# Kernel optimization log

Hardware: AMD Instinct MI355X
Metric: run time of the kernel (lower is better)

## Reference

```python
import jax, jax.numpy as jnp
import numpy as np

N_NODES = 100000
N_EDGES = 1600000
DIM = 128
N_LAYERS = 3   # num_gc_layers
N_RES = 3      # residual VQ layers
N_CODE = 16    # codebook_size
N_GRAPHS = 512
BN_EPS = 1e-5
COMMIT_W = 0.25


def _l2norm(v):
    return v * jax.lax.rsqrt(jnp.sum(v * v, axis=-1, keepdims=True) + 1e-12)


def setup_inputs() -> dict:
    key = jax.random.key(0)
    ks = jax.random.split(key, 8)
    s = 0.05
    x = jax.random.normal(ks[0], (N_NODES, DIM), jnp.float32)
    edge_index = jax.random.randint(ks[1], (2, N_EDGES), 0, N_NODES)
    batch = jnp.sort(jax.random.randint(ks[2], (N_NODES,), 0, N_GRAPHS))
    W1 = jax.random.normal(ks[3], (N_LAYERS, DIM, DIM), jnp.float32) * s
    b1 = jnp.zeros((N_LAYERS, DIM), jnp.float32)
    W2 = jax.random.normal(ks[4], (N_LAYERS, DIM, DIM), jnp.float32) * s
    b2 = jnp.zeros((N_LAYERS, DIM), jnp.float32)
    gamma = jnp.ones((N_LAYERS, DIM), jnp.float32)
    beta = jnp.zeros((N_LAYERS, DIM), jnp.float32)
    codebooks = jax.random.normal(ks[5], (N_LAYERS, N_RES, N_CODE, DIM), jnp.float32)
    return dict(x=x, edge_index=edge_index, batch=batch, W1=W1, b1=b1,
                W2=W2, b2=b2, gamma=gamma, beta=beta, codebooks=codebooks)


def reference(x, edge_index, batch, W1, b1, W2, b2, gamma, beta, codebooks):
    src, dst = edge_index[0], edge_index[1]
    h = x
    xs, ids = [], []
    commit_loss = jnp.float32(0.0)
    for i in range(N_LAYERS):
        # GINConv, eps=0: MLP((1+eps)*x + sum_{j->i} x_j)
        agg = jax.ops.segment_sum(h[src], dst, num_segments=N_NODES)
        h = agg + h
        h = jax.nn.relu(h @ W1[i] + b1[i]) @ W2[i] + b2[i]  # Linear-ReLU-Linear
        h = jax.nn.relu(h)                                   # outer F.relu
        # BatchNorm1d (training-mode batch stats, biased variance)
        mean = jnp.mean(h, axis=0)
        var = jnp.var(h, axis=0)
        h = (h - mean) * jax.lax.rsqrt(var + BN_EPS) * gamma[i] + beta[i]
        xs.append(h)
        # Residual VQ with cosine-sim codebook (3 residual layers)
        r = h
        lids = []
        for l in range(N_RES):
            cbn = _l2norm(codebooks[i, l])           # [K, D] normalized codebook
            sim = _l2norm(r) @ cbn.T                  # [N, K] cosine similarity
            idx = jnp.argmax(sim, axis=-1)            # nearest code
            q = cbn[idx]                              # quantized residual
            commit_loss = commit_loss + COMMIT_W * jnp.mean(
                (jax.lax.stop_gradient(q) - r) ** 2)
            r = r - jax.lax.stop_gradient(q)
            lids.append(idx)
        ids.append(jnp.stack(lids, axis=1))           # [N, N_RES]
    xs_cat = jnp.concatenate(xs, axis=1)              # [N, DIM*N_LAYERS]
    xpool = jax.ops.segment_sum(xs_cat, batch, num_segments=N_GRAPHS)
    id_cat = jnp.concatenate(ids, axis=1)             # [N, N_RES*N_LAYERS]
    return xpool, xs_cat, commit_loss, id_cat
```

## Files before the change

kernel.cpp:

```cpp
#include <hip/hip_runtime.h>
#include <hip/hip_bf16.h>

#define N_NODES 100000
#define N_EDGES 1600000
#define DIM 128
#define NLAY 3
#define NRES 3
#define NCODE 16
#define NGRAPH 512
#define SCAN_NB ((N_NODES + 255) / 256)
#define GEMM_NB ((N_NODES + 63) / 64)

using bf16 = __hip_bfloat16;

__device__ inline void atomAddD(double* p, double v) { unsafeAtomicAdd(p, v); }

__device__ inline double ldx(const void* p, long i, int isbf) {
  if (isbf) return (double)__bfloat162float(((const bf16*)p)[i]);
  return (double)((const float*)p)[i];
}
__device__ inline void stout(void* p, long i, double v, int isbf) {
  if (isbf) ((bf16*)p)[i] = __float2bfloat16((float)v);
  else ((float*)p)[i] = (float)v;
}

__global__ void k_detect(const unsigned int* __restrict__ x, int* __restrict__ flag) {
  int tid = threadIdx.x;
  int cnt = 0;
  for (int j = tid; j < 1024; j += 256) {
    unsigned int u = x[j];
    int e = (u >> 7) & 0xFF;
    cnt += (e >= 100 && e <= 135) ? 1 : 0;
  }
  __shared__ int sh[256];
  sh[tid] = cnt; __syncthreads();
  for (int s = 128; s; s >>= 1) { if (tid < s) sh[tid] += sh[tid + s]; __syncthreads(); }
  if (tid == 0) flag[0] = (sh[0] > 512) ? 1 : 0;
}

__global__ __launch_bounds__(256) void k_convert_f(const void* __restrict__ x, float* __restrict__ hf,
                                                   long n, const int* __restrict__ flag) {
  int isbf = flag[0];
  long i = (long)blockIdx.x * 256 + threadIdx.x;
  if (i < n) hf[i] = (float)ldx(x, i, isbf);
}

__global__ __launch_bounds__(256) void k_hist(const int* __restrict__ ei, int* __restrict__ deg) {
  int e = blockIdx.x * 256 + threadIdx.x;
  if (e < N_EDGES) atomicAdd(&deg[ei[N_EDGES + e]], 1);
}

__global__ __launch_bounds__(256) void k_scan1(const int* __restrict__ deg, int* __restrict__ bsum) {
  int i = blockIdx.x * 256 + threadIdx.x;
  int v = (i < N_NODES) ? deg[i] : 0;
  for (int o = 32; o; o >>= 1) v += __shfl_xor(v, o);
  __shared__ int sh[4];
  if ((threadIdx.x & 63) == 0) sh[threadIdx.x >> 6] = v;
  __syncthreads();
  if (threadIdx.x == 0) bsum[blockIdx.x] = sh[0] + sh[1] + sh[2] + sh[3];
}

__global__ void k_scan2(int* __restrict__ bsum) {
  __shared__ int sh[512];
  int t = threadIdx.x;
  int v = (t < SCAN_NB) ? bsum[t] : 0;
  sh[t] = v; __syncthreads();
  for (int s = 1; s < 512; s <<= 1) {
    int add = (t >= s) ? sh[t - s] : 0;
    __syncthreads();
    sh[t] += add;
    __syncthreads();
  }
  if (t < SCAN_NB) bsum[t] = sh[t] - v;
}

__global__ __launch_bounds__(256) void k_scan3(const int* __restrict__ deg, const int* __restrict__ bsum,
                                               int* __restrict__ ofs, int* __restrict__ cursor) {
  int t = threadIdx.x;
  int i = blockIdx.x * 256 + t;
  int v = (i < N_NODES) ? deg[i] : 0;
  __shared__ int sh[256];
  sh[t] = v; __syncthreads();
  for (int s = 1; s < 256; s <<= 1) {
    int add = (t >= s) ? sh[t - s] : 0;
    __syncthreads();
    sh[t] += add;
    __syncthreads();
  }
  int excl = sh[t] - v + bsum[blockIdx.x];
  if (i < N_NODES) { ofs[i] = excl; cursor[i] = excl; }
  if (i == N_NODES - 1) ofs[N_NODES] = excl + v;
}

__global__ __launch_bounds__(256) void k_fill(const int* __restrict__ ei, int* __restrict__ cursor,
                                              int* __restrict__ csr) {
  int e = blockIdx.x * 256 + threadIdx.x;
  if (e < N_EDGES) {
    int d = ei[N_EDGES + e];
    int p = atomicAdd(&cursor[d], 1);
    csr[p] = ei[e];
  }
}

__global__ __launch_bounds__(256) void k_gather(const float* __restrict__ hf,
                                                const int* __restrict__ ofs,
                                                const int* __restrict__ csr,
                                                float* __restrict__ outQ) {
  int node = blockIdx.x * 4 + (threadIdx.x >> 6);
  int lane = threadIdx.x & 63;
  int beg = ofs[node], end = ofs[node + 1];
  float2 sv = *(const float2*)&hf[(long)node * DIM + lane * 2];
  double accx = (double)sv.x, accy = (double)sv.y;
  int j = beg;
  for (; j + 3 < end; j += 4) {
    int s0 = csr[j], s1 = csr[j + 1], s2 = csr[j + 2], s3 = csr[j + 3];
    float2 v0 = *(const float2*)&hf[(long)s0 * DIM + lane * 2];
    float2 v1 = *(const float2*)&hf[(long)s1 * DIM + lane * 2];
    float2 v2 = *(const float2*)&hf[(long)s2 * DIM + lane * 2];
    float2 v3 = *(const float2*)&hf[(long)s3 * DIM + lane * 2];
    accx += (double)v0.x; accy += (double)v0.y;
    accx += (double)v1.x; accy += (double)v1.y;
    accx += (double)v2.x; accy += (double)v2.y;
    accx += (double)v3.x; accy += (double)v3.y;
  }
  for (; j < end; j++) {
    int s0 = csr[j];
    float2 v0 = *(const float2*)&hf[(long)s0 * DIM + lane * 2];
    accx += (double)v0.x; accy += (double)v0.y;
  }
  *(float2*)&outQ[(long)node * DIM + lane * 2] = make_float2((float)accx, (float)accy);
}

__global__ void k_cbn(const void* __restrict__ cb, double* __restrict__ cbn, const int* __restrict__ flag) {
  int isbf = flag[0];
  int b = blockIdx.x, d = threadIdx.x;
  double v0 = ldx(cb, (long)b * DIM + d, isbf);
  double v1 = ldx(cb, (long)b * DIM + d + 64, isbf);
  double ss = v0 * v0 + v1 * v1;
  for (int o = 32; o; o >>= 1) ss += __shfl_xor(ss, o);
  double inv = 1.0 / sqrt(ss + 1e-12);
  cbn[b * DIM + d] = v0 * inv;
  cbn[b * DIM + d + 64] = v1 * inv;
}

__global__ void k_gram(const double* __restrict__ cbn, double* __restrict__ G) {
  int b = blockIdx.x, t = threadIdx.x;
  int l = b / (48 * 48); int rem = b % (48 * 48); int a = rem / 48, c = rem % 48;
  const double* ra = cbn + (long)(l * 48 + a) * DIM;
  const double* rc = cbn + (long)(l * 48 + c) * DIM;
  double s = ra[t] * rc[t] + ra[t + 64] * rc[t + 64];
  for (int o = 32; o; o >>= 1) s += __shfl_xor(s, o);
  if (t == 0) G[b] = s;
}

__global__ __launch_bounds__(256) void k_gemm_relu_f(const float* __restrict__ in,
                                                     const float* __restrict__ W,
                                                     const float* __restrict__ bias,
                                                     float* __restrict__ out) {
  __shared__ float ul[64 * DIM];
  int tid = threadIdx.x;
  long base = (long)blockIdx.x * 64;
  for (int j = tid; j < 64 * DIM / 4; j += 256) {
    long row = base + (j >> 5);
    float4 v = make_float4(0.f, 0.f, 0.f, 0.f);
    if (row < N_NODES) v = *(const float4*)&in[base * DIM + (long)j * 4];
    *(float4*)&ul[j * 4] = v;
  }
  __syncthreads();
  int cl = tid & 31;
  int rw = tid >> 5;
  int c0 = cl * 4;
  float acc[8][4] = {};
  for (int k = 0; k < DIM; k += 4) {
    float4 w0 = *(const float4*)&W[(k + 0) * DIM + c0];
    float4 w1 = *(const float4*)&W[(k + 1) * DIM + c0];
    float4 w2 = *(const float4*)&W[(k + 2) * DIM + c0];
    float4 w3 = *(const float4*)&W[(k + 3) * DIM + c0];
#pragma unroll
    for (int r = 0; r < 8; r++) {
      float4 u = *(const float4*)&ul[(rw * 8 + r) * DIM + k];
      acc[r][0] += u.x * w0.x + u.y * w1.x + u.z * w2.x + u.w * w3.x;
      acc[r][1] += u.x * w0.y + u.y * w1.y + u.z * w2.y + u.w * w3.y;
      acc[r][2] += u.x * w0.z + u.y * w1.z + u.z * w2.z + u.w * w3.z;
      acc[r][3] += u.x * w0.w + u.y * w1.w + u.z * w2.w + u.w * w3.w;
    }
  }
  float4 bv = *(const float4*)&bias[c0];
#pragma unroll
  for (int r = 0; r < 8; r++) {
    long row = base + rw * 8 + r;
    if (row < N_NODES) {
      float4 o;
      o.x = fmaxf(acc[r][0] + bv.x, 0.f);
      o.y = fmaxf(acc[r][1] + bv.y, 0.f);
      o.z = fmaxf(acc[r][2] + bv.z, 0.f);
      o.w = fmaxf(acc[r][3] + bv.w, 0.f);
      *(float4*)&out[row * DIM + c0] = o;
    }
  }
}

__global__ __launch_bounds__(256) void k_gemm_relu_stats(const float* __restrict__ in,
                                                         const float* __restrict__ W,
                                                         const float* __restrict__ bias,
                                                         float* __restrict__ out,
                                                         double* __restrict__ stats8) {
  __shared__ __align__(16) float ul[64 * DIM];
  int tid = threadIdx.x;
  long base = (long)blockIdx.x * 64;
  for (int j = tid; j < 64 * DIM / 4; j += 256) {
    long row = base + (j >> 5);
    float4 v = make_float4(0.f, 0.f, 0.f, 0.f);
    if (row < N_NODES) v = *(const float4*)&in[base * DIM + (long)j * 4];
    *(float4*)&ul[j * 4] = v;
  }
  __syncthreads();
  int cl = tid & 31;
  int rw = tid >> 5;
  int c0 = cl * 4;
  float acc[8][4] = {};
  for (int k = 0; k < DIM; k += 4) {
    float4 w0 = *(const float4*)&W[(k + 0) * DIM + c0];
    float4 w1 = *(const float4*)&W[(k + 1) * DIM + c0];
    float4 w2 = *(const float4*)&W[(k + 2) * DIM + c0];
    float4 w3 = *(const float4*)&W[(k + 3) * DIM + c0];
#pragma unroll
    for (int r = 0; r < 8; r++) {
      float4 u = *(const float4*)&ul[(rw * 8 + r) * DIM + k];
      acc[r][0] += u.x * w0.x + u.y * w1.x + u.z * w2.x + u.w * w3.x;
      acc[r][1] += u.x * w0.y + u.y * w1.y + u.z * w2.y + u.w * w3.y;
      acc[r][2] += u.x * w0.z + u.y * w1.z + u.z * w2.z + u.w * w3.z;
      acc[r][3] += u.x * w0.w + u.y * w1.w + u.z * w2.w + u.w * w3.w;
    }
  }
  float4 bv = *(const float4*)&bias[c0];
  double cs0 = 0.0, cs1 = 0.0, cs2 = 0.0, cs3 = 0.0;
  double q0 = 0.0, q1 = 0.0, q2 = 0.0, q3 = 0.0;
#pragma unroll
  for (int r = 0; r < 8; r++) {
    long row = base + rw * 8 + r;
    if (row < N_NODES) {
      float4 o;
      o.x = fmaxf(acc[r][0] + bv.x, 0.f);
      o.y = fmaxf(acc[r][1] + bv.y, 0.f);
      o.z = fmaxf(acc[r][2] + bv.z, 0.f);
      o.w = fmaxf(acc[r][3] + bv.w, 0.f);
      *(float4*)&out[row * DIM + c0] = o;
      double dx = (double)o.x, dy = (double)o.y, dz = (double)o.z, dw = (double)o.w;
      cs0 += dx; q0 += dx * dx;
      cs1 += dy; q1 += dy * dy;
      cs2 += dz; q2 += dz * dz;
      cs3 += dw; q3 += dw * dw;
    }
  }
  __syncthreads();
  double* sred = (double*)ul;
  sred[rw * 128 + c0 + 0] = cs0; sred[1024 + rw * 128 + c0 + 0] = q0;
  sred[rw * 128 + c0 + 1] = cs1; sred[1024 + rw * 128 + c0 + 1] = q1;
  sred[rw * 128 + c0 + 2] = cs2; sred[1024 + rw * 128 + c0 + 2] = q2;
  sred[rw * 128 + c0 + 3] = cs3; sred[1024 + rw * 128 + c0 + 3] = q3;
  __syncthreads();
  if (tid < 128) {
    double S = 0.0, S2 = 0.0;
#pragma unroll
    for (int i = 0; i < 8; i++) { S += sred[i * 128 + tid]; S2 += sred[1024 + i * 128 + tid]; }
    int slab = blockIdx.x & 7;
    atomAddD(&stats8[slab * 256 + tid], S);
    atomAddD(&stats8[slab * 256 + 128 + tid], S2);
  }
}

__global__ __launch_bounds__(256) void k_post(float* __restrict__ h,
                                              const double* __restrict__ stats8,
                                              const void* __restrict__ gamma,
                                              const void* __restrict__ beta,
                                              const int* __restrict__ batch,
                                              void* __restrict__ out,
                                              double* __restrict__ xpool,
                                              double* __restrict__ hh,
                                              int l, const int* __restrict__ flag) {
  __shared__ float hl[64 * 132];
  __shared__ double hq[64 * 4];
  __shared__ double ssl[256];
  __shared__ int sbat[64];
  int isbf = flag[0];
  int tid = threadIdx.x;
  long base = (long)blockIdx.x * 64;
  if (tid < 128) {
    double sum = 0.0, sumsq = 0.0;
#pragma unroll
    for (int s8 = 0; s8 < 8; s8++) { sum += stats8[s8 * 256 + tid]; sumsq += stats8[s8 * 256 + 128 + tid]; }
    double mean = sum / (double)N_NODES;
    double var = sumsq / (double)N_NODES - mean * mean;
    double sc = ldx(gamma, (long)l * DIM + tid, isbf) / sqrt(var + 1e-5);
    ssl[tid] = sc;
    ssl[DIM + tid] = ldx(beta, (long)l * DIM + tid, isbf) - mean * sc;
  }
  if (tid < 64) {
    long row = base + tid;
    sbat[tid] = (row < N_NODES) ? batch[row] : -1;
  }
  __syncthreads();
  int d = tid & 127, half = tid >> 7;
  double sc = ssl[d], sh = ssl[DIM + d];
  const long XS_BASE = (long)NGRAPH * DIM * NLAY;
  for (int rr = half; rr < 64; rr += 2) {
    long row = base + rr;
    float vf = 0.f;
    if (row < N_NODES) {
      double v = (double)h[row * DIM + d] * sc + sh;
      vf = (float)v;
      h[row * DIM + d] = vf;
      stout(out, XS_BASE + row * (DIM * NLAY) + l * DIM + d, v, isbf);
    }
    hl[rr * 132 + d] = vf;
  }
  __syncthreads();
  {
    int row = tid >> 2, q = tid & 3;
    double s2 = 0.0;
    const float* hp = &hl[row * 132 + q * 32];
#pragma unroll
    for (int i = 0; i < 32; i++) { double v = (double)hp[i]; s2 += v * v; }
    hq[row * 4 + q] = s2;
  }
  __syncthreads();
  if (tid < 64) {
    long n = base + tid;
    if (n < N_NODES) hh[n] = hq[tid * 4] + hq[tid * 4 + 1] + hq[tid * 4 + 2] + hq[tid * 4 + 3];
  } else if (tid >= 128) {
    int dd = tid - 128;
    int g = sbat[0];
    double acc = 0.0;
    for (int r = 0; r < 64; r++) {
      int gg = sbat[r];
      if (gg < 0) break;
      if (gg != g) {
        atomAddD(&xpool[(long)g * (DIM * NLAY) + l * DIM + dd], acc);
        acc = 0.0; g = gg;
      }
      acc += (double)hl[r * 132 + dd];
    }
    atomAddD(&xpool[(long)g * (DIM * NLAY) + l * DIM + dd], acc);
  }
}

__global__ __launch_bounds__(256) void k_dotH(const float* __restrict__ hn,
                                              const double* __restrict__ cbnL,
                                              float* __restrict__ dH) {
  __shared__ double cl[48 * 134];
  int tid = threadIdx.x;
  for (int j = tid; j < 48 * DIM; j += 256) { int c = j >> 7, k = j & 127; cl[c * 134 + k] = cbnL[j]; }
  __syncthreads();
  int ct = tid & 7; int c0 = ct * 6; int rt = tid >> 3;
  long r0 = (long)blockIdx.x * 64 + rt; long r1 = r0 + 32;
  long r0c = r0 < N_NODES ? r0 : (N_NODES - 1);
  long r1c = r1 < N_NODES ? r1 : (N_NODES - 1);
  double acc0[6] = {}, acc1[6] = {};
  for (int k = 0; k < DIM; k += 4) {
    float4 h0 = *(const float4*)&hn[r0c * DIM + k];
    float4 h1 = *(const float4*)&hn[r1c * DIM + k];
#pragma unroll
    for (int j = 0; j < 6; j++) {
      double2 ca = *(const double2*)&cl[(c0 + j) * 134 + k];
      double2 cb = *(const double2*)&cl[(c0 + j) * 134 + k + 2];
      acc0[j] += (double)h0.x * ca.x + (double)h0.y * ca.y + (double)h0.z * cb.x + (double)h0.w * cb.y;
      acc1[j] += (double)h1.x * ca.x + (double)h1.y * ca.y + (double)h1.z * cb.x + (double)h1.w * cb.y;
    }
  }
  if (r0 < N_NODES) {
#pragma unroll
    for (int j = 0; j < 6; j++) dH[r0 * 48 + c0 + j] = (float)acc0[j];
  }
  if (r1 < N_NODES) {
#pragma unroll
    for (int j = 0; j < 6; j++) dH[r1 * 48 + c0 + j] = (float)acc1[j];
  }
}

__global__ __launch_bounds__(256) void k_vq(const float* __restrict__ dH, const double* __restrict__ hh,
                                            const double* __restrict__ G, void* __restrict__ out,
                                            double* __restrict__ commit, int l, const int* __restrict__ flag) {
  int isbf = flag[0];
  __shared__ double Gl[48 * 48];
  int tid = threadIdx.x;
  for (int j = tid; j < 48 * 48; j += 256) Gl[j] = G[j];
  __syncthreads();
  long n = (long)blockIdx.x * 256 + tid;
  double csum = 0.0;
  if (n < N_NODES) {
    double dh[48];
#pragma unroll
    for (int c = 0; c < 48; c++) dh[c] = (double)dH[n * 48 + c];
    int i0 = 0; double b0 = dh[0];
#pragma unroll
    for (int c = 1; c < 16; c++) { if (dh[c] > b0) { b0 = dh[c]; i0 = c; } }
    int i1 = 0; double b1 = dh[16] - Gl[i0 * 48 + 16];
#pragma unroll
    for (int c = 1; c < 16; c++) {
      double s = dh[16 + c] - Gl[i0 * 48 + 16 + c];
      if (s > b1) { b1 = s; i1 = c; }
    }
    int i2 = 0; double b2 = dh[32] - Gl[i0 * 48 + 32] - Gl[(16 + i1) * 48 + 32];
#pragma unroll
    for (int c = 1; c < 16; c++) {
      double s = dh[32 + c] - Gl[i0 * 48 + 32 + c] - Gl[(16 + i1) * 48 + 32 + c];
      if (s > b2) { b2 = s; i2 = c; }
    }
    double r1s = hh[n] - 2.0 * b0 + Gl[i0 * 48 + i0];
    double r2s = r1s - 2.0 * b1 + Gl[(16 + i1) * 48 + 16 + i1];
    double r3s = r2s - 2.0 * b2 + Gl[(32 + i2) * 48 + 32 + i2];
    csum = r1s + r2s + r3s;
    const long IDS_BASE = (long)NGRAPH * DIM * NLAY + (long)N_NODES * DIM * NLAY + 1;
    long base = IDS_BASE + n * (NLAY * NRES) + l * NRES;
    stout(out, base + 0, (double)i0, isbf);
    stout(out, base + 1, (double)i1, isbf);
    stout(out, base + 2, (double)i2, isbf);
  }
  for (int o = 32; o; o >>= 1) csum += __shfl_xor(csum, o);
  if ((tid & 63) == 0 && csum != 0.0) atomAddD(commit, csum);
}

__global__ __launch_bounds__(256) void k_out(const double* __restrict__ xpool, const double* __restrict__ commit,
                                             void* __restrict__ out, const int* __restrict__ flag) {
  int isbf = flag[0];
  long i = (long)blockIdx.x * 256 + threadIdx.x;
  const long NP = (long)NGRAPH * DIM * NLAY;
  if (i < NP) {
    stout(out, i, xpool[i], isbf);
  } else if (i == NP) {
    double c = commit[0] * (0.25 / ((double)N_NODES * (double)DIM));
    stout(out, NP + (long)N_NODES * DIM * NLAY, c, isbf);
  }
}

extern "C" void kernel_launch(void* const* d_in, const int* in_sizes, int n_in,
                              void* d_out, int out_size, void* d_ws, size_t ws_size,
                              hipStream_t stream) {
  const void* x = d_in[0];
  const int* ei = (const int*)d_in[1];
  const int* batch = (const int*)d_in[2];
  const void* W1 = d_in[3];
  const void* b1 = d_in[4];
  const void* W2 = d_in[5];
  const void* b2 = d_in[6];
  const void* gamma = d_in[7];
  const void* beta = d_in[8];
  const void* cb = d_in[9];

  double* w = (double*)d_ws;
  double* cbn = w;
  double* G = cbn + 18432;
  double* stats8 = G + 6912;
  double* hh = stats8 + 2048;
  double* xpool = hh + N_NODES;
  double* commit = xpool + (long)NGRAPH * DIM * NLAY;
  float* W1f = (float*)(commit + 2);
  float* W2f = W1f + 49152;
  float* b1f = W2f + 49152;
  float* b2f = b1f + 384;
  float* H  = b2f + 384;
  float* T1 = H + 12800000;
  float* T2 = T1 + 12800000;
  float* dH = T2 + 12800000;
  int* ibuf = (int*)(dH + 4800000);
  int* flag = ibuf;
  int* deg = ibuf + 64;
  int* ofs = deg + N_NODES;
  int* cursor = ofs + N_NODES + 1;
  int* csr = cursor + N_NODES;
  int* bsum = csr + N_EDGES;

  k_detect<<<1, 256, 0, stream>>>((const unsigned int*)x, flag);
  hipMemsetAsync(xpool, 0, ((long)NGRAPH * DIM * NLAY + 1) * sizeof(double), stream);
  hipMemsetAsync(deg, 0, N_NODES * sizeof(int), stream);
  k_convert_f<<<50000, 256, 0, stream>>>(x, H, (long)N_NODES * DIM, flag);
  k_convert_f<<<192, 256, 0, stream>>>(W1, W1f, 49152, flag);
  k_convert_f<<<192, 256, 0, stream>>>(W2, W2f, 49152, flag);
  k_convert_f<<<2, 256, 0, stream>>>(b1, b1f, 384, flag);
  k_convert_f<<<2, 256, 0, stream>>>(b2, b2f, 384, flag);
  k_cbn<<<NLAY * NRES * NCODE, 64, 0, stream>>>(cb, cbn, flag);
  k_gram<<<NLAY * 48 * 48, 64, 0, stream>>>(cbn, G);
  k_hist<<<(N_EDGES + 255) / 256, 256, 0, stream>>>(ei, deg);
  k_scan1<<<SCAN_NB, 256, 0, stream>>>(deg, bsum);
  k_scan2<<<1, 512, 0, stream>>>(bsum);
  k_scan3<<<SCAN_NB, 256, 0, stream>>>(deg, bsum, ofs, cursor);
  k_fill<<<(N_EDGES + 255) / 256, 256, 0, stream>>>(ei, cursor, csr);

  for (int l = 0; l < NLAY; l++) {
    k_gather<<<N_NODES / 4, 256, 0, stream>>>(H, ofs, csr, T1);
    k_gemm_relu_f<<<GEMM_NB, 256, 0, stream>>>(T1, W1f + l * DIM * DIM, b1f + l * DIM, T2);
    hipMemsetAsync(stats8, 0, 2048 * sizeof(double), stream);
    k_gemm_relu_stats<<<GEMM_NB, 256, 0, stream>>>(T2, W2f + l * DIM * DIM, b2f + l * DIM, T1, stats8);
    k_post<<<GEMM_NB, 256, 0, stream>>>(T1, stats8, gamma, beta, batch, d_out, xpool, hh, l, flag);
    k_dotH<<<1563, 256, 0, stream>>>(T1, cbn + (long)l * 48 * DIM, dH);
    k_vq<<<391, 256, 0, stream>>>(dH, hh, G + l * 48 * 48, d_out, commit, l, flag);
    float* t = H; H = T1; T1 = t;
  }
  k_out<<<769, 256, 0, stream>>>(xpool, commit, d_out, flag);
}
```

Measured before the change: 1.597 ms.

## Fuse MLP GEMMs into one kernel and gather directly from raw input

Merges the two Linear layers into one kernel that keeps the ReLU intermediate in shared memory, avoiding a full write and read of the hidden tensor per layer. The first layer gathers straight from the input tensor (bf16 or fp32), removing the separate conversion pass. The stats buffer is zeroed inside the gather kernel instead of with a memset. The fused kernel does twice the compute per block with extra barriers.

```diff
diff --git a/kernel.cpp b/kernel.cpp
--- a/kernel.cpp
+++ b/kernel.cpp
@@ -105,7 +105,9 @@
 __global__ __launch_bounds__(256) void k_gather(const float* __restrict__ hf,
                                                 const int* __restrict__ ofs,
                                                 const int* __restrict__ csr,
-                                                float* __restrict__ outQ) {
+                                                float* __restrict__ outQ,
+                                                double* __restrict__ stats8) {
+  if (blockIdx.x < 8) stats8[blockIdx.x * 256 + threadIdx.x] = 0.0;
   int node = blockIdx.x * 4 + (threadIdx.x >> 6);
   int lane = threadIdx.x & 63;
   int beg = ofs[node], end = ofs[node + 1];
@@ -131,6 +133,65 @@
   *(float2*)&outQ[(long)node * DIM + lane * 2] = make_float2((float)accx, (float)accy);
 }
 
+__global__ __launch_bounds__(256) void k_gather_x(const void* __restrict__ x,
+                                                  const int* __restrict__ ofs,
+                                                  const int* __restrict__ csr,
+                                                  float* __restrict__ outQ,
+                                                  double* __restrict__ stats8,
+                                                  const int* __restrict__ flag) {
+  if (blockIdx.x < 8) stats8[blockIdx.x * 256 + threadIdx.x] = 0.0;
+  int isbf = flag[0];
+  int node = blockIdx.x * 4 + (threadIdx.x >> 6);
+  int lane = threadIdx.x & 63;
+  int beg = ofs[node], end = ofs[node + 1];
+  double accx, accy;
+  if (isbf) {
+    const unsigned short* xb = (const unsigned short*)x;
+    unsigned int u = *(const unsigned int*)&xb[(long)node * DIM + lane * 2];
+    accx = (double)__uint_as_float(u << 16);
+    accy = (double)__uint_as_float(u & 0xffff0000u);
+    int j = beg;
+    for (; j + 3 < end; j += 4) {
+      int s0 = csr[j], s1 = csr[j + 1], s2 = csr[j + 2], s3 = csr[j + 3];
+      unsigned int u0 = *(const unsigned int*)&xb[(long)s0 * DIM + lane * 2];
+      unsigned int u1 = *(const unsigned int*)&xb[(long)s1 * DIM + lane * 2];
+      unsigned int u2 = *(const unsigned int*)&xb[(long)s2 * DIM + lane * 2];
+      unsigned int u3 = *(const unsigned int*)&xb[(long)s3 * DIM + lane * 2];
+      accx += (double)__uint_as_float(u0 << 16); accy += (double)__uint_as_float(u0 & 0xffff0000u);
+      accx += (double)__uint_as_float(u1 << 16); accy += (double)__uint_as_float(u1 & 0xffff0000u);
+      accx += (double)__uint_as_float(u2 << 16); accy += (double)__uint_as_float(u2 & 0xffff0000u);
+      accx += (double)__uint_as_float(u3 << 16); accy += (double)__uint_as_float(u3 & 0xffff0000u);
+    }
+    for (; j < end; j++) {
+      int s0 = csr[j];
+      unsigned int u0 = *(const unsigned int*)&xb[(long)s0 * DIM + lane * 2];
+      accx += (double)__uint_as_float(u0 << 16); accy += (double)__uint_as_float(u0 & 0xffff0000u);
+    }
+  } else {
+    const float* hf = (const float*)x;
+    float2 sv = *(const float2*)&hf[(long)node * DIM + lane * 2];
+    accx = (double)sv.x; accy = (double)sv.y;
+    int j = beg;
+    for (; j + 3 < end; j += 4) {
+      int s0 = csr[j], s1 = csr[j + 1], s2 = csr[j + 2], s3 = csr[j + 3];
+      float2 v0 = *(const float2*)&hf[(long)s0 * DIM + lane * 2];
+      float2 v1 = *(const float2*)&hf[(long)s1 * DIM + lane * 2];
+      float2 v2 = *(const float2*)&hf[(long)s2 * DIM + lane * 2];
+      float2 v3 = *(const float2*)&hf[(long)s3 * DIM + lane * 2];
+      accx += (double)v0.x; accy += (double)v0.y;
+      accx += (double)v1.x; accy += (double)v1.y;
+      accx += (double)v2.x; accy += (double)v2.y;
+      accx += (double)v3.x; accy += (double)v3.y;
+    }
+    for (; j < end; j++) {
+      int s0 = csr[j];
+      float2 v0 = *(const float2*)&hf[(long)s0 * DIM + lane * 2];
+      accx += (double)v0.x; accy += (double)v0.y;
+    }
+  }
+  *(float2*)&outQ[(long)node * DIM + lane * 2] = make_float2((float)accx, (float)accy);
+}
+
 __global__ void k_cbn(const void* __restrict__ cb, double* __restrict__ cbn, const int* __restrict__ flag) {
   int isbf = flag[0];
   int b = blockIdx.x, d = threadIdx.x;
@@ -153,58 +214,13 @@
   if (t == 0) G[b] = s;
 }
 
-__global__ __launch_bounds__(256) void k_gemm_relu_f(const float* __restrict__ in,
-                                                     const float* __restrict__ W,
-                                                     const float* __restrict__ bias,
-                                                     float* __restrict__ out) {
-  __shared__ float ul[64 * DIM];
-  int tid = threadIdx.x;
-  long base = (long)blockIdx.x * 64;
-  for (int j = tid; j < 64 * DIM / 4; j += 256) {
-    long row = base + (j >> 5);
-    float4 v = make_float4(0.f, 0.f, 0.f, 0.f);
-    if (row < N_NODES) v = *(const float4*)&in[base * DIM + (long)j * 4];
-    *(float4*)&ul[j * 4] = v;
-  }
-  __syncthreads();
-  int cl = tid & 31;
-  int rw = tid >> 5;
-  int c0 = cl * 4;
-  float acc[8][4] = {};
-  for (int k = 0; k < DIM; k += 4) {
-    float4 w0 = *(const float4*)&W[(k + 0) * DIM + c0];
-    float4 w1 = *(const float4*)&W[(k + 1) * DIM + c0];
-    float4 w2 = *(const float4*)&W[(k + 2) * DIM + c0];
-    float4 w3 = *(const float4*)&W[(k + 3) * DIM + c0];
-#pragma unroll
-    for (int r = 0; r < 8; r++) {
-      float4 u = *(const float4*)&ul[(rw * 8 + r) * DIM + k];
-      acc[r][0] += u.x * w0.x + u.y * w1.x + u.z * w2.x + u.w * w3.x;
-      acc[r][1] += u.x * w0.y + u.y * w1.y + u.z * w2.y + u.w * w3.y;
-      acc[r][2] += u.x * w0.z + u.y * w1.z + u.z * w2.z + u.w * w3.z;
-      acc[r][3] += u.x * w0.w + u.y * w1.w + u.z * w2.w + u.w * w3.w;
-    }
-  }
-  float4 bv = *(const float4*)&bias[c0];
-#pragma unroll
-  for (int r = 0; r < 8; r++) {
-    long row = base + rw * 8 + r;
-    if (row < N_NODES) {
-      float4 o;
-      o.x = fmaxf(acc[r][0] + bv.x, 0.f);
-      o.y = fmaxf(acc[r][1] + bv.y, 0.f);
-      o.z = fmaxf(acc[r][2] + bv.z, 0.f);
-      o.w = fmaxf(acc[r][3] + bv.w, 0.f);
-      *(float4*)&out[row * DIM + c0] = o;
-    }
-  }
-}
-
-__global__ __launch_bounds__(256) void k_gemm_relu_stats(const float* __restrict__ in,
-                                                         const float* __restrict__ W,
-                                                         const float* __restrict__ bias,
-                                                         float* __restrict__ out,
-                                                         double* __restrict__ stats8) {
+__global__ __launch_bounds__(256) void k_gemm_pair(const float* __restrict__ in,
+                                                   const float* __restrict__ W1g,
+                                                   const float* __restrict__ b1g,
+                                                   const float* __restrict__ W2g,
+                                                   const float* __restrict__ b2g,
+                                                   float* __restrict__ out,
+                                                   double* __restrict__ stats8) {
   __shared__ __align__(16) float ul[64 * DIM];
   int tid = threadIdx.x;
   long base = (long)blockIdx.x * 64;
@@ -220,10 +236,10 @@
   int c0 = cl * 4;
   float acc[8][4] = {};
   for (int k = 0; k < DIM; k += 4) {
-    float4 w0 = *(const float4*)&W[(k + 0) * DIM + c0];
-    float4 w1 = *(const float4*)&W[(k + 1) * DIM + c0];
-    float4 w2 = *(const float4*)&W[(k + 2) * DIM + c0];
-    float4 w3 = *(const float4*)&W[(k + 3) * DIM + c0];
+    float4 w0 = *(const float4*)&W1g[(k + 0) * DIM + c0];
+    float4 w1 = *(const float4*)&W1g[(k + 1) * DIM + c0];
+    float4 w2 = *(const float4*)&W1g[(k + 2) * DIM + c0];
+    float4 w3 = *(const float4*)&W1g[(k + 3) * DIM + c0];
 #pragma unroll
     for (int r = 0; r < 8; r++) {
       float4 u = *(const float4*)&ul[(rw * 8 + r) * DIM + k];
@@ -233,7 +249,38 @@
       acc[r][3] += u.x * w0.w + u.y * w1.w + u.z * w2.w + u.w * w3.w;
     }
   }
-  float4 bv = *(const float4*)&bias[c0];
+  {
+    float4 bv = *(const float4*)&b1g[c0];
+#pragma unroll
+    for (int r = 0; r < 8; r++) {
+      acc[r][0] = fmaxf(acc[r][0] + bv.x, 0.f);
+      acc[r][1] = fmaxf(acc[r][1] + bv.y, 0.f);
+      acc[r][2] = fmaxf(acc[r][2] + bv.z, 0.f);
+      acc[r][3] = fmaxf(acc[r][3] + bv.w, 0.f);
+    }
+  }
+  __syncthreads();
+#pragma unroll
+  for (int r = 0; r < 8; r++)
+    *(float4*)&ul[(rw * 8 + r) * DIM + c0] = make_float4(acc[r][0], acc[r][1], acc[r][2], acc[r][3]);
+  __syncthreads();
+#pragma unroll
+  for (int r = 0; r < 8; r++) { acc[r][0] = 0.f; acc[r][1] = 0.f; acc[r][2] = 0.f; acc[r][3] = 0.f; }
+  for (int k = 0; k < DIM; k += 4) {
+    float4 w0 = *(const float4*)&W2g[(k + 0) * DIM + c0];
+    float4 w1 = *(const float4*)&W2g[(k + 1) * DIM + c0];
+    float4 w2 = *(const float4*)&W2g[(k + 2) * DIM + c0];
+    float4 w3 = *(const float4*)&W2g[(k + 3) * DIM + c0];
+#pragma unroll
+    for (int r = 0; r < 8; r++) {
+      float4 u = *(const float4*)&ul[(rw * 8 + r) * DIM + k];
+      acc[r][0] += u.x * w0.x + u.y * w1.x + u.z * w2.x + u.w * w3.x;
+      acc[r][1] += u.x * w0.y + u.y * w1.y + u.z * w2.y + u.w * w3.y;
+      acc[r][2] += u.x * w0.z + u.y * w1.z + u.z * w2.z + u.w * w3.z;
+      acc[r][3] += u.x * w0.w + u.y * w1.w + u.z * w2.w + u.w * w3.w;
+    }
+  }
+  float4 bv = *(const float4*)&b2g[c0];
   double cs0 = 0.0, cs1 = 0.0, cs2 = 0.0, cs3 = 0.0;
   double q0 = 0.0, q1 = 0.0, q2 = 0.0, q3 = 0.0;
 #pragma unroll
@@ -459,10 +506,10 @@
   float* W2f = W1f + 49152;
   float* b1f = W2f + 49152;
   float* b2f = b1f + 384;
-  float* H  = b2f + 384;
-  float* T1 = H + 12800000;
-  float* T2 = T1 + 12800000;
-  float* dH = T2 + 12800000;
+  float* buf0 = b2f + 384;
+  float* buf1 = buf0 + 12800000;
+  float* buf2 = buf1 + 12800000;
+  float* dH = buf2 + 12800000;
   int* ibuf = (int*)(dH + 4800000);
   int* flag = ibuf;
   int* deg = ibuf + 64;
@@ -474,7 +521,6 @@
   k_detect<<<1, 256, 0, stream>>>((const unsigned int*)x, flag);
   hipMemsetAsync(xpool, 0, ((long)NGRAPH * DIM * NLAY + 1) * sizeof(double), stream);
   hipMemsetAsync(deg, 0, N_NODES * sizeof(int), stream);
-  k_convert_f<<<50000, 256, 0, stream>>>(x, H, (long)N_NODES * DIM, flag);
   k_convert_f<<<192, 256, 0, stream>>>(W1, W1f, 49152, flag);
   k_convert_f<<<192, 256, 0, stream>>>(W2, W2f, 49152, flag);
   k_convert_f<<<2, 256, 0, stream>>>(b1, b1f, 384, flag);
@@ -487,15 +533,19 @@
   k_scan3<<<SCAN_NB, 256, 0, stream>>>(deg, bsum, ofs, cursor);
   k_fill<<<(N_EDGES + 255) / 256, 256, 0, stream>>>(ei, cursor, csr);
 
+  float* Hcur = nullptr;
   for (int l = 0; l < NLAY; l++) {
-    k_gather<<<N_NODES / 4, 256, 0, stream>>>(H, ofs, csr, T1);
-    k_gemm_relu_f<<<GEMM_NB, 256, 0, stream>>>(T1, W1f + l * DIM * DIM, b1f + l * DIM, T2);
-    hipMemsetAsync(stats8, 0, 2048 * sizeof(double), stream);
-    k_gemm_relu_stats<<<GEMM_NB, 256, 0, stream>>>(T2, W2f + l * DIM * DIM, b2f + l * DIM, T1, stats8);
-    k_post<<<GEMM_NB, 256, 0, stream>>>(T1, stats8, gamma, beta, batch, d_out, xpool, hh, l, flag);
-    k_dotH<<<1563, 256, 0, stream>>>(T1, cbn + (long)l * 48 * DIM, dH);
+    float* PO = (l & 1) ? buf2 : buf1;
+    if (l == 0)
+      k_gather_x<<<N_NODES / 4, 256, 0, stream>>>(x, ofs, csr, buf0, stats8, flag);
+    else
+      k_gather<<<N_NODES / 4, 256, 0, stream>>>(Hcur, ofs, csr, buf0, stats8);
+    k_gemm_pair<<<GEMM_NB, 256, 0, stream>>>(buf0, W1f + l * DIM * DIM, b1f + l * DIM,
+                                             W2f + l * DIM * DIM, b2f + l * DIM, PO, stats8);
+    k_post<<<GEMM_NB, 256, 0, stream>>>(PO, stats8, gamma, beta, batch, d_out, xpool, hh, l, flag);
+    k_dotH<<<1563, 256, 0, stream>>>(PO, cbn + (long)l * 48 * DIM, dH);
     k_vq<<<391, 256, 0, stream>>>(dH, hh, G + l * 48 * 48, d_out, commit, l, flag);
-    float* t = H; H = T1; T1 = t;
+    Hcur = PO;
   }
   k_out<<<769, 256, 0, stream>>>(xpool, commit, d_out, flag);
 }
```

New measurement: 1.527 ms. 4.4% less time.
